# Kernel optimization log

Measured on AMD Instinct MI355X. Metric: run time of the kernel, lower is better.

Reference implementation:

```python
import jax, jax.numpy as jnp
import numpy as np

N_WORDS, N_SENTS = 200_000, 20_000
IN_DIM, OUT_DIM, FEAT = 128, 64, 50
N_EDGES = 2_000_000
NEG_SLOPE = 0.01  # torch F.leaky_relu default


def setup_inputs() -> dict:
    key = jax.random.key(0)
    k = jax.random.split(key, 7)
    h = jax.random.normal(k[0], (N_WORDS + N_SENTS, IN_DIM), dtype=jnp.float32)
    tfidf = jax.random.normal(k[1], (N_EDGES, FEAT), dtype=jnp.float32)
    W_fc = jax.random.normal(k[2], (OUT_DIM, IN_DIM), dtype=jnp.float32) / np.sqrt(IN_DIM)
    W_feat = jax.random.normal(k[3], (OUT_DIM, FEAT), dtype=jnp.float32) / np.sqrt(FEAT)
    W_attn = jax.random.normal(k[4], (1, 3 * OUT_DIM), dtype=jnp.float32) / np.sqrt(3 * OUT_DIM)
    src = jax.random.randint(k[5], (N_EDGES,), 0, N_WORDS, dtype=jnp.int32)
    dst = jax.random.randint(k[6], (N_EDGES,), 0, N_SENTS, dtype=jnp.int32)
    return {"h": h, "tfidf": tfidf, "W_fc": W_fc, "W_feat": W_feat,
            "W_attn": W_attn, "src": src, "dst": dst, "n_sents": N_SENTS}


def reference(h, tfidf, W_fc, W_feat, W_attn, src, dst, n_sents):
    n_words = h.shape[0] - n_sents
    out_dim = W_fc.shape[0]
    z = h @ W_fc.T                                  # [N, D]
    z_src = z[src]                                  # [E, D] gather word z
    z_dst = z[n_words + dst]                        # [E, D] gather sentence z
    dfeat = tfidf @ W_feat.T                        # [E, D] feat_fc
    wa = W_attn[0]                                  # [3D]; concat+linear == split dot
    e = z_src @ wa[:out_dim] + z_dst @ wa[out_dim:2 * out_dim] + dfeat @ wa[2 * out_dim:]
    e = jnp.where(e >= 0, e, NEG_SLOPE * e)         # leaky_relu, [E]
    # segment softmax over each sentence's incoming edges
    m = jax.ops.segment_max(e, dst, num_segments=n_sents)
    m = jnp.where(jnp.isfinite(m), m, 0.0)          # guard empty segments
    ex = jnp.exp(e - m[dst])
    denom = jax.ops.segment_sum(ex, dst, num_segments=n_sents)
    alpha = ex / denom[dst]                         # [E]
    # weighted scatter-sum of source features
    sh = jax.ops.segment_sum(alpha[:, None] * z_src, dst, num_segments=n_sents)
    return sh                                       # [n_sents, D]
```

## Files before the change

### kernel.cpp

```cpp
#include <hip/hip_runtime.h>
#include <hip/hip_bf16.h>
#include <hip/hip_fp16.h>
#include <cstdint>

#define IN_DIM 128
#define OUT_DIM 64
#define FEATD 50
#define NEG_SLOPE 0.01f

typedef unsigned int uint32;
typedef _Float16 half4 __attribute__((ext_vector_type(4)));
typedef float f32x4 __attribute__((ext_vector_type(4)));

__global__ __launch_bounds__(256) void k_v3zero(const float* __restrict__ W_feat,
                                                const float* __restrict__ W_attn,
                                                float* __restrict__ v3,
                                                uint32* __restrict__ cnt,
                                                int n_sents) {
  int i = blockIdx.x * 256 + threadIdx.x;
  if (i < n_sents) cnt[i] = 0u;
  if (blockIdx.x == 0 && threadIdx.x < FEATD) {
    int j = threadIdx.x;
    float s = 0.f;
    #pragma unroll
    for (int o = 0; o < OUT_DIM; ++o)
      s = fmaf(W_attn[2 * OUT_DIM + o], W_feat[o * FEATD + j], s);
    v3[j] = s;
  }
}

__global__ __launch_bounds__(256) void k_node_mfma(const float* __restrict__ h,
    const float* __restrict__ W_fc, const float* __restrict__ W_attn,
    __half* __restrict__ z, float* __restrict__ s1, float* __restrict__ s2,
    int n_words, int n_nodes) {
  __shared__ float zl[4][16][68];
  int w = threadIdx.x >> 6, lane = threadIdx.x & 63;
  int nb = blockIdx.x * 64 + w * 16;
  int lrow = lane & 15;
  int lk4 = (lane >> 4) * 4;

  int an = nb + lrow;
  if (an >= n_nodes) an = n_nodes - 1;
  const float* hrow = h + (size_t)an * IN_DIM;

  f32x4 acc[4];
  #pragma unroll
  for (int nt = 0; nt < 4; ++nt) acc[nt] = (f32x4){0.f, 0.f, 0.f, 0.f};

  #pragma unroll
  for (int ks = 0; ks < 8; ++ks) {
    float4 hv = *(const float4*)(hrow + ks * 16 + lk4);
    half4 a;
    a[0] = (_Float16)hv.x; a[1] = (_Float16)hv.y;
    a[2] = (_Float16)hv.z; a[3] = (_Float16)hv.w;
    #pragma unroll
    for (int nt = 0; nt < 4; ++nt) {
      const float* wrow = W_fc + (size_t)(nt * 16 + lrow) * IN_DIM + ks * 16 + lk4;
      float4 wv = *(const float4*)wrow;
      half4 b;
      b[0] = (_Float16)wv.x; b[1] = (_Float16)wv.y;
      b[2] = (_Float16)wv.z; b[3] = (_Float16)wv.w;
      acc[nt] = __builtin_amdgcn_mfma_f32_16x16x16f16(a, b, acc[nt], 0, 0, 0);
    }
  }

  int drow = (lane >> 4) * 4;
  #pragma unroll
  for (int nt = 0; nt < 4; ++nt)
    #pragma unroll
    for (int r = 0; r < 4; ++r)
      zl[w][drow + r][nt * 16 + lrow] = acc[nt][r];

  int node = lane >> 2;
  int chunk = lane & 3;
  float v[16];
  #pragma unroll
  for (int q = 0; q < 4; ++q) {
    float4 t = *(const float4*)&zl[w][node][chunk * 16 + q * 4];
    v[4 * q + 0] = t.x; v[4 * q + 1] = t.y;
    v[4 * q + 2] = t.z; v[4 * q + 3] = t.w;
  }

  int gn = nb + node;
  bool valid = gn < n_nodes;
  bool isword = gn < n_words;
  const float* wa = W_attn + (isword ? 0 : OUT_DIM) + chunk * 16;
  float p = 0.f;
  #pragma unroll
  for (int t = 0; t < 16; ++t) p = fmaf(v[t], wa[t], p);
  p += __shfl_xor(p, 1);
  p += __shfl_xor(p, 2);

  if (valid && chunk == 0) {
    if (isword) s1[gn] = p; else s2[gn - n_words] = p;
  }
  if (valid && isword) {
    uint32 d[8];
    #pragma unroll
    for (int k = 0; k < 8; ++k) {
      __half2 t = __floats2half2_rn(v[2 * k], v[2 * k + 1]);
      d[k] = *(uint32*)&t;
    }
    uint4* dst = (uint4*)(z + (size_t)gn * OUT_DIM + chunk * 16);
    dst[0] = make_uint4(d[0], d[1], d[2], d[3]);
    dst[1] = make_uint4(d[4], d[5], d[6], d[7]);
  }
}

__global__ __launch_bounds__(256) void k_hist(const int* __restrict__ dst,
                                              uint32* __restrict__ cnt,
                                              uint32* __restrict__ rank, int E) {
  int e = blockIdx.x * 256 + threadIdx.x;
  if (e < E) rank[e] = atomicAdd(&cnt[dst[e]], 1u);
}

__global__ __launch_bounds__(1024) void k_scan(const uint32* __restrict__ cnt,
    uint32* __restrict__ off, int n) {
  __shared__ uint32 part[1024];
  int t = threadIdx.x;
  int CH = (n + 1023) >> 10;
  int base = t * CH;
  uint32 s = 0;
  for (int k = 0; k < CH; ++k) { int i = base + k; if (i < n) s += cnt[i]; }
  part[t] = s;
  __syncthreads();
  uint32 x = s;
  for (int d = 1; d < 1024; d <<= 1) {
    uint32 v = (t >= d) ? part[t - d] : 0u;
    __syncthreads();
    x += v;
    part[t] = x;
    __syncthreads();
  }
  uint32 run = (t > 0) ? part[t - 1] : 0u;
  for (int k = 0; k < CH; ++k) {
    int i = base + k;
    if (i < n) { off[i] = run; run += cnt[i]; }
  }
  if (t == 1023) off[n] = part[1023];
}

__global__ __launch_bounds__(256) void k_edge(const float* __restrict__ tfidf,
    const int* __restrict__ src, const int* __restrict__ dst,
    const float* __restrict__ s1, const float* __restrict__ s2,
    const float* __restrict__ v3, const uint32* __restrict__ off,
    const uint32* __restrict__ rank, float2* __restrict__ pair, int E) {
  int e = blockIdx.x * 256 + threadIdx.x;
  if (e >= E) return;
  const float* row = tfidf + (size_t)e * FEATD;
  float f = 0.f;
  #pragma unroll
  for (int k = 0; k < FEATD / 2; ++k) {
    float2 v = *(const float2*)(row + 2 * k);
    f = fmaf(v.x, v3[2 * k], f);
    f = fmaf(v.y, v3[2 * k + 1], f);
  }
  int sidx = src[e], d = dst[e];
  float ev = s1[sidx] + s2[d] + f;
  ev = ev >= 0.f ? ev : NEG_SLOPE * ev;
  float exv = __expf(ev);
  float2 pr;
  pr.x = exv;
  pr.y = __int_as_float(sidx);
  pair[off[d] + rank[e]] = pr;
}

__global__ __launch_bounds__(256) void k_agg(const __half* __restrict__ z,
    const float2* __restrict__ pair, const uint32* __restrict__ off,
    float* __restrict__ out, int n_sents) {
  int w = threadIdx.x >> 6, lane = threadIdx.x & 63;
  int s = blockIdx.x * 4 + w;
  if (s >= n_sents) return;
  uint32 j0 = off[s], j1 = off[s + 1];

  float acc = 0.f, sa = 0.f;
  uint32 j = j0;
  for (; j + 8 <= j1; j += 8) {
    float2 p[8];
    #pragma unroll
    for (int k = 0; k < 8; ++k) p[k] = pair[j + k];
    float v[8];
    #pragma unroll
    for (int k = 0; k < 8; ++k)
      v[k] = __half2float(z[(size_t)(uint32)__float_as_int(p[k].y) * OUT_DIM + lane]);
    #pragma unroll
    for (int k = 0; k < 8; ++k) { acc = fmaf(p[k].x, v[k], acc); sa += p[k].x; }
  }
  for (; j + 4 <= j1; j += 4) {
    float2 p[4];
    #pragma unroll
    for (int k = 0; k < 4; ++k) p[k] = pair[j + k];
    float v[4];
    #pragma unroll
    for (int k = 0; k < 4; ++k)
      v[k] = __half2float(z[(size_t)(uint32)__float_as_int(p[k].y) * OUT_DIM + lane]);
    #pragma unroll
    for (int k = 0; k < 4; ++k) { acc = fmaf(p[k].x, v[k], acc); sa += p[k].x; }
  }
  for (; j < j1; ++j) {
    float2 p = pair[j];
    float v = __half2float(z[(size_t)(uint32)__float_as_int(p.y) * OUT_DIM + lane]);
    acc = fmaf(p.x, v, acc);
    sa += p.x;
  }

  out[(size_t)s * OUT_DIM + lane] = (sa > 0.f) ? (acc / sa) : 0.f;
}

extern "C" void kernel_launch(void* const* d_in, const int* in_sizes, int n_in,
                              void* d_out, int out_size, void* d_ws, size_t ws_size,
                              hipStream_t stream) {
  const float* h      = (const float*)d_in[0];
  const float* tfidf  = (const float*)d_in[1];
  const float* W_fc   = (const float*)d_in[2];
  const float* W_feat = (const float*)d_in[3];
  const float* W_attn = (const float*)d_in[4];
  const int*   src    = (const int*)d_in[5];
  const int*   dst    = (const int*)d_in[6];

  int n_nodes = in_sizes[0] / IN_DIM;
  int E       = in_sizes[5];
  int n_sents = out_size / OUT_DIM;
  int n_words = n_nodes - n_sents;
  float* out = (float*)d_out;

  char* ws = (char*)d_ws;
  size_t ofs = 0;
  auto alloc = [&](size_t bytes) -> char* {
    char* p = ws + ofs;
    ofs += (bytes + 255) / 256 * 256;
    return p;
  };
  __half* z      = (__half*)alloc((size_t)n_words * OUT_DIM * 2);
  float*  s1     = (float*)alloc((size_t)n_words * 4);
  float*  s2     = (float*)alloc((size_t)n_sents * 4);
  float2* pair   = (float2*)alloc((size_t)E * 8);
  uint32* rank   = (uint32*)alloc((size_t)E * 4);
  uint32* cnt    = (uint32*)alloc((size_t)n_sents * 4);
  uint32* offs   = (uint32*)alloc((size_t)(n_sents + 1) * 4);
  float*  v3     = (float*)alloc(FEATD * 4);
  (void)ws_size; (void)n_in;

  k_v3zero<<<(n_sents + 255) / 256, 256, 0, stream>>>(W_feat, W_attn, v3, cnt,
                                                      n_sents);
  k_node_mfma<<<(n_nodes + 63) / 64, 256, 0, stream>>>(h, W_fc, W_attn, z, s1,
                                                       s2, n_words, n_nodes);
  k_hist<<<(E + 255) / 256, 256, 0, stream>>>(dst, cnt, rank, E);
  k_scan<<<1, 1024, 0, stream>>>(cnt, offs, n_sents);
  k_edge<<<(E + 255) / 256, 256, 0, stream>>>(tfidf, src, dst, s1, s2, v3,
                                              offs, rank, pair, E);
  k_agg<<<(n_sents + 3) / 4, 256, 0, stream>>>(z, pair, offs, out, n_sents);
}
```

Measured before the change: 422.7 us.

## Fuse histogram into node GEMM launch and split edge dot across four lanes

Merges the dst histogram/rank atomics into the node MFMA kernel as extra blocks, so the two independent phases share one launch and can overlap. Each histogram thread now handles two edges with a vectorized int2 load. The edge kernel spreads each 50-wide tfidf dot product over four lanes with a shuffle reduction, so consecutive lanes read adjacent addresses instead of striding by 200 bytes. The cost is that three of every four lanes sit idle during the scatter tail, and the grid is four times larger.

```diff
diff --git a/kernel.cpp b/kernel.cpp
--- a/kernel.cpp
+++ b/kernel.cpp
@@ -29,11 +29,26 @@
   }
 }
 
-__global__ __launch_bounds__(256) void k_node_mfma(const float* __restrict__ h,
+__global__ __launch_bounds__(256) void k_node_hist(const float* __restrict__ h,
     const float* __restrict__ W_fc, const float* __restrict__ W_attn,
     __half* __restrict__ z, float* __restrict__ s1, float* __restrict__ s2,
-    int n_words, int n_nodes) {
+    const int* __restrict__ dst, uint32* __restrict__ cnt,
+    uint32* __restrict__ rank, int n_words, int n_nodes, int node_blocks,
+    int E) {
   __shared__ float zl[4][16][68];
+  if (blockIdx.x >= node_blocks) {
+    int i = (blockIdx.x - node_blocks) * 256 + threadIdx.x;
+    int e0 = i * 2;
+    if (e0 + 1 < E) {
+      int2 d2 = *(const int2*)(dst + e0);
+      uint32 r0 = atomicAdd(&cnt[d2.x], 1u);
+      uint32 r1 = atomicAdd(&cnt[d2.y], 1u);
+      *(uint2*)(rank + e0) = make_uint2(r0, r1);
+    } else if (e0 < E) {
+      rank[e0] = atomicAdd(&cnt[dst[e0]], 1u);
+    }
+    return;
+  }
   int w = threadIdx.x >> 6, lane = threadIdx.x & 63;
   int nb = blockIdx.x * 64 + w * 16;
   int lrow = lane & 15;
@@ -101,17 +116,10 @@
       __half2 t = __floats2half2_rn(v[2 * k], v[2 * k + 1]);
       d[k] = *(uint32*)&t;
     }
-    uint4* dst = (uint4*)(z + (size_t)gn * OUT_DIM + chunk * 16);
-    dst[0] = make_uint4(d[0], d[1], d[2], d[3]);
-    dst[1] = make_uint4(d[4], d[5], d[6], d[7]);
-  }
-}
-
-__global__ __launch_bounds__(256) void k_hist(const int* __restrict__ dst,
-                                              uint32* __restrict__ cnt,
-                                              uint32* __restrict__ rank, int E) {
-  int e = blockIdx.x * 256 + threadIdx.x;
-  if (e < E) rank[e] = atomicAdd(&cnt[dst[e]], 1u);
+    uint4* dstp = (uint4*)(z + (size_t)gn * OUT_DIM + chunk * 16);
+    dstp[0] = make_uint4(d[0], d[1], d[2], d[3]);
+    dstp[1] = make_uint4(d[4], d[5], d[6], d[7]);
+  }
 }
 
 __global__ __launch_bounds__(1024) void k_scan(const uint32* __restrict__ cnt,
@@ -145,24 +153,37 @@
     const float* __restrict__ s1, const float* __restrict__ s2,
     const float* __restrict__ v3, const uint32* __restrict__ off,
     const uint32* __restrict__ rank, float2* __restrict__ pair, int E) {
-  int e = blockIdx.x * 256 + threadIdx.x;
+  int t = threadIdx.x;
+  int g = t >> 2, r = t & 3;
+  int e = blockIdx.x * 64 + g;
   if (e >= E) return;
-  const float* row = tfidf + (size_t)e * FEATD;
+  const float2* row2 = (const float2*)(tfidf + (size_t)e * FEATD);
+  const float2* v32 = (const float2*)v3;
   float f = 0.f;
   #pragma unroll
-  for (int k = 0; k < FEATD / 2; ++k) {
-    float2 v = *(const float2*)(row + 2 * k);
-    f = fmaf(v.x, v3[2 * k], f);
-    f = fmaf(v.y, v3[2 * k + 1], f);
-  }
-  int sidx = src[e], d = dst[e];
-  float ev = s1[sidx] + s2[d] + f;
-  ev = ev >= 0.f ? ev : NEG_SLOPE * ev;
-  float exv = __expf(ev);
-  float2 pr;
-  pr.x = exv;
-  pr.y = __int_as_float(sidx);
-  pair[off[d] + rank[e]] = pr;
+  for (int q = 0; q < 6; ++q) {
+    float2 v = row2[r + 4 * q];
+    float2 c = v32[r + 4 * q];
+    f = fmaf(v.x, c.x, f);
+    f = fmaf(v.y, c.y, f);
+  }
+  if (r == 0) {
+    float2 v = row2[24];
+    float2 c = v32[24];
+    f = fmaf(v.x, c.x, f);
+    f = fmaf(v.y, c.y, f);
+  }
+  f += __shfl_xor(f, 1);
+  f += __shfl_xor(f, 2);
+  if (r == 0) {
+    int sidx = src[e], d = dst[e];
+    float ev = s1[sidx] + s2[d] + f;
+    ev = ev >= 0.f ? ev : NEG_SLOPE * ev;
+    float2 pr;
+    pr.x = __expf(ev);
+    pr.y = __int_as_float(sidx);
+    pair[off[d] + rank[e]] = pr;
+  }
 }
 
 __global__ __launch_bounds__(256) void k_agg(const __half* __restrict__ z,
@@ -241,13 +262,16 @@
   float*  v3     = (float*)alloc(FEATD * 4);
   (void)ws_size; (void)n_in;
 
+  int node_blocks = (n_nodes + 63) / 64;
+  int hist_blocks = (E + 511) / 512;
+
   k_v3zero<<<(n_sents + 255) / 256, 256, 0, stream>>>(W_feat, W_attn, v3, cnt,
                                                       n_sents);
-  k_node_mfma<<<(n_nodes + 63) / 64, 256, 0, stream>>>(h, W_fc, W_attn, z, s1,
-                                                       s2, n_words, n_nodes);
-  k_hist<<<(E + 255) / 256, 256, 0, stream>>>(dst, cnt, rank, E);
+  k_node_hist<<<node_blocks + hist_blocks, 256, 0, stream>>>(
+      h, W_fc, W_attn, z, s1, s2, dst, cnt, rank, n_words, n_nodes,
+      node_blocks, E);
   k_scan<<<1, 1024, 0, stream>>>(cnt, offs, n_sents);
-  k_edge<<<(E + 255) / 256, 256, 0, stream>>>(tfidf, src, dst, s1, s2, v3,
-                                              offs, rank, pair, E);
+  k_edge<<<(E + 63) / 64, 256, 0, stream>>>(tfidf, src, dst, s1, s2, v3,
+                                            offs, rank, pair, E);
   k_agg<<<(n_sents + 3) / 4, 256, 0, stream>>>(z, pair, offs, out, n_sents);
 }
```

Result: no change. 430.5 us (+1.8%).

## Split aggregation into source-sorted scatter of weighted rows and contiguous reduce

Applied to the files above, without the earlier changes.

Edges are additionally bucketed by source word, so each word's z row is loaded once and multiplied by its edge weights. The weighted rows are scattered into a per-edge half buffer ordered by destination, which the sentence reduction then reads contiguously. This is meant to replace random z gathers in aggregation with streaming reads. In exchange it adds a second atomic histogram and scan, and a very large intermediate buffer that must be written and read.

```diff
diff --git a/kernel.cpp b/kernel.cpp
--- a/kernel.cpp
+++ b/kernel.cpp
@@ -12,13 +12,15 @@
 typedef _Float16 half4 __attribute__((ext_vector_type(4)));
 typedef float f32x4 __attribute__((ext_vector_type(4)));
 
-__global__ __launch_bounds__(256) void k_v3zero(const float* __restrict__ W_feat,
-                                                const float* __restrict__ W_attn,
-                                                float* __restrict__ v3,
-                                                uint32* __restrict__ cnt,
-                                                int n_sents) {
+__global__ __launch_bounds__(256) void k_init(const float* __restrict__ W_feat,
+                                              const float* __restrict__ W_attn,
+                                              float* __restrict__ v3,
+                                              uint32* __restrict__ cnt_d,
+                                              uint32* __restrict__ cnt_s,
+                                              int n_sents, int n_words) {
   int i = blockIdx.x * 256 + threadIdx.x;
-  if (i < n_sents) cnt[i] = 0u;
+  if (i < n_sents) cnt_d[i] = 0u;
+  if (i < n_words) cnt_s[i] = 0u;
   if (blockIdx.x == 0 && threadIdx.x < FEATD) {
     int j = threadIdx.x;
     float s = 0.f;
@@ -101,21 +103,32 @@
       __half2 t = __floats2half2_rn(v[2 * k], v[2 * k + 1]);
       d[k] = *(uint32*)&t;
     }
-    uint4* dst = (uint4*)(z + (size_t)gn * OUT_DIM + chunk * 16);
-    dst[0] = make_uint4(d[0], d[1], d[2], d[3]);
-    dst[1] = make_uint4(d[4], d[5], d[6], d[7]);
-  }
-}
-
-__global__ __launch_bounds__(256) void k_hist(const int* __restrict__ dst,
-                                              uint32* __restrict__ cnt,
-                                              uint32* __restrict__ rank, int E) {
+    uint4* dstp = (uint4*)(z + (size_t)gn * OUT_DIM + chunk * 16);
+    dstp[0] = make_uint4(d[0], d[1], d[2], d[3]);
+    dstp[1] = make_uint4(d[4], d[5], d[6], d[7]);
+  }
+}
+
+__global__ __launch_bounds__(256) void k_hist2(const int* __restrict__ dst,
+                                               const int* __restrict__ src,
+                                               uint32* __restrict__ cnt_d,
+                                               uint32* __restrict__ cnt_s,
+                                               uint32* __restrict__ rank_d,
+                                               uint32* __restrict__ rank_s,
+                                               int E) {
   int e = blockIdx.x * 256 + threadIdx.x;
-  if (e < E) rank[e] = atomicAdd(&cnt[dst[e]], 1u);
-}
-
-__global__ __launch_bounds__(1024) void k_scan(const uint32* __restrict__ cnt,
-    uint32* __restrict__ off, int n) {
+  if (e < E) {
+    rank_d[e] = atomicAdd(&cnt_d[dst[e]], 1u);
+    rank_s[e] = atomicAdd(&cnt_s[src[e]], 1u);
+  }
+}
+
+__global__ __launch_bounds__(1024) void k_scan2(const uint32* __restrict__ cnt_d,
+    uint32* __restrict__ off_d, int nd, const uint32* __restrict__ cnt_s,
+    uint32* __restrict__ off_s, int ns) {
+  const uint32* cnt = (blockIdx.x == 0) ? cnt_d : cnt_s;
+  uint32* off = (blockIdx.x == 0) ? off_d : off_s;
+  int n = (blockIdx.x == 0) ? nd : ns;
   __shared__ uint32 part[1024];
   int t = threadIdx.x;
   int CH = (n + 1023) >> 10;
@@ -143,8 +156,10 @@
 __global__ __launch_bounds__(256) void k_edge(const float* __restrict__ tfidf,
     const int* __restrict__ src, const int* __restrict__ dst,
     const float* __restrict__ s1, const float* __restrict__ s2,
-    const float* __restrict__ v3, const uint32* __restrict__ off,
-    const uint32* __restrict__ rank, float2* __restrict__ pair, int E) {
+    const float* __restrict__ v3, const uint32* __restrict__ off_d,
+    const uint32* __restrict__ off_s, const uint32* __restrict__ rank_d,
+    const uint32* __restrict__ rank_s, float* __restrict__ aw,
+    float2* __restrict__ asd, int E) {
   int e = blockIdx.x * 256 + threadIdx.x;
   if (e >= E) return;
   const float* row = tfidf + (size_t)e * FEATD;
@@ -159,51 +174,62 @@
   float ev = s1[sidx] + s2[d] + f;
   ev = ev >= 0.f ? ev : NEG_SLOPE * ev;
   float exv = __expf(ev);
+  uint32 sd = off_d[d] + rank_d[e];
+  uint32 ss = off_s[sidx] + rank_s[e];
+  aw[sd] = exv;
   float2 pr;
   pr.x = exv;
-  pr.y = __int_as_float(sidx);
-  pair[off[d] + rank[e]] = pr;
-}
-
-__global__ __launch_bounds__(256) void k_agg(const __half* __restrict__ z,
-    const float2* __restrict__ pair, const uint32* __restrict__ off,
+  pr.y = __int_as_float((int)sd);
+  asd[ss] = pr;
+}
+
+__global__ __launch_bounds__(256) void k_pv(const __half* __restrict__ z,
+    const float2* __restrict__ asd, const uint32* __restrict__ off_s,
+    __half* __restrict__ wbuf, int n_words) {
+  int w = blockIdx.x * 4 + (threadIdx.x >> 6);
+  int lane = threadIdx.x & 63;
+  if (w >= n_words) return;
+  float zv = __half2float(z[(size_t)w * OUT_DIM + lane]);
+  uint32 j0 = off_s[w], j1 = off_s[w + 1];
+  uint32 j = j0;
+  for (; j + 2 <= j1; j += 2) {
+    float2 a0 = asd[j];
+    float2 a1 = asd[j + 1];
+    uint32 t0 = (uint32)__float_as_int(a0.y);
+    uint32 t1 = (uint32)__float_as_int(a1.y);
+    wbuf[(size_t)t0 * OUT_DIM + lane] = __float2half(a0.x * zv);
+    wbuf[(size_t)t1 * OUT_DIM + lane] = __float2half(a1.x * zv);
+  }
+  if (j < j1) {
+    float2 a0 = asd[j];
+    uint32 t0 = (uint32)__float_as_int(a0.y);
+    wbuf[(size_t)t0 * OUT_DIM + lane] = __float2half(a0.x * zv);
+  }
+}
+
+__global__ __launch_bounds__(256) void k_aggB(const __half* __restrict__ wbuf,
+    const float* __restrict__ aw, const uint32* __restrict__ off_d,
     float* __restrict__ out, int n_sents) {
-  int w = threadIdx.x >> 6, lane = threadIdx.x & 63;
-  int s = blockIdx.x * 4 + w;
+  int s = blockIdx.x * 4 + (threadIdx.x >> 6);
+  int lane = threadIdx.x & 63;
   if (s >= n_sents) return;
-  uint32 j0 = off[s], j1 = off[s + 1];
-
+  uint32 j0 = off_d[s], j1 = off_d[s + 1];
   float acc = 0.f, sa = 0.f;
   uint32 j = j0;
   for (; j + 8 <= j1; j += 8) {
-    float2 p[8];
-    #pragma unroll
-    for (int k = 0; k < 8; ++k) p[k] = pair[j + k];
-    float v[8];
-    #pragma unroll
-    for (int k = 0; k < 8; ++k)
-      v[k] = __half2float(z[(size_t)(uint32)__float_as_int(p[k].y) * OUT_DIM + lane]);
-    #pragma unroll
-    for (int k = 0; k < 8; ++k) { acc = fmaf(p[k].x, v[k], acc); sa += p[k].x; }
-  }
-  for (; j + 4 <= j1; j += 4) {
-    float2 p[4];
-    #pragma unroll
-    for (int k = 0; k < 4; ++k) p[k] = pair[j + k];
-    float v[4];
-    #pragma unroll
-    for (int k = 0; k < 4; ++k)
-      v[k] = __half2float(z[(size_t)(uint32)__float_as_int(p[k].y) * OUT_DIM + lane]);
-    #pragma unroll
-    for (int k = 0; k < 4; ++k) { acc = fmaf(p[k].x, v[k], acc); sa += p[k].x; }
+    __half hv[8];
+    float av[8];
+    #pragma unroll
+    for (int k = 0; k < 8; ++k) hv[k] = wbuf[(size_t)(j + k) * OUT_DIM + lane];
+    #pragma unroll
+    for (int k = 0; k < 8; ++k) av[k] = aw[j + k];
+    #pragma unroll
+    for (int k = 0; k < 8; ++k) { acc += __half2float(hv[k]); sa += av[k]; }
   }
   for (; j < j1; ++j) {
-    float2 p = pair[j];
-    float v = __half2float(z[(size_t)(uint32)__float_as_int(p.y) * OUT_DIM + lane]);
-    acc = fmaf(p.x, v, acc);
-    sa += p.x;
-  }
-
+    acc += __half2float(wbuf[(size_t)j * OUT_DIM + lane]);
+    sa += aw[j];
+  }
   out[(size_t)s * OUT_DIM + lane] = (sa > 0.f) ? (acc / sa) : 0.f;
 }
 
@@ -234,20 +260,28 @@
   __half* z      = (__half*)alloc((size_t)n_words * OUT_DIM * 2);
   float*  s1     = (float*)alloc((size_t)n_words * 4);
   float*  s2     = (float*)alloc((size_t)n_sents * 4);
-  float2* pair   = (float2*)alloc((size_t)E * 8);
-  uint32* rank   = (uint32*)alloc((size_t)E * 4);
-  uint32* cnt    = (uint32*)alloc((size_t)n_sents * 4);
-  uint32* offs   = (uint32*)alloc((size_t)(n_sents + 1) * 4);
+  __half* wbuf   = (__half*)alloc((size_t)E * OUT_DIM * 2);
+  float2* asd    = (float2*)alloc((size_t)E * 8);
+  float*  aw     = (float*)alloc((size_t)E * 4);
+  uint32* rank_d = (uint32*)alloc((size_t)E * 4);
+  uint32* rank_s = (uint32*)alloc((size_t)E * 4);
+  uint32* cnt_d  = (uint32*)alloc((size_t)n_sents * 4);
+  uint32* cnt_s  = (uint32*)alloc((size_t)n_words * 4);
+  uint32* off_d  = (uint32*)alloc((size_t)(n_sents + 1) * 4);
+  uint32* off_s  = (uint32*)alloc((size_t)(n_words + 1) * 4);
   float*  v3     = (float*)alloc(FEATD * 4);
   (void)ws_size; (void)n_in;
 
-  k_v3zero<<<(n_sents + 255) / 256, 256, 0, stream>>>(W_feat, W_attn, v3, cnt,
-                                                      n_sents);
+  k_init<<<(n_words + 255) / 256, 256, 0, stream>>>(W_feat, W_attn, v3, cnt_d,
+                                                    cnt_s, n_sents, n_words);
   k_node_mfma<<<(n_nodes + 63) / 64, 256, 0, stream>>>(h, W_fc, W_attn, z, s1,
                                                        s2, n_words, n_nodes);
-  k_hist<<<(E + 255) / 256, 256, 0, stream>>>(dst, cnt, rank, E);
-  k_scan<<<1, 1024, 0, stream>>>(cnt, offs, n_sents);
+  k_hist2<<<(E + 255) / 256, 256, 0, stream>>>(dst, src, cnt_d, cnt_s, rank_d,
+                                               rank_s, E);
+  k_scan2<<<2, 1024, 0, stream>>>(cnt_d, off_d, n_sents, cnt_s, off_s, n_words);
   k_edge<<<(E + 255) / 256, 256, 0, stream>>>(tfidf, src, dst, s1, s2, v3,
-                                              offs, rank, pair, E);
-  k_agg<<<(n_sents + 3) / 4, 256, 0, stream>>>(z, pair, offs, out, n_sents);
-}
+                                              off_d, off_s, rank_d, rank_s,
+                                              aw, asd, E);
+  k_pv<<<(n_words + 3) / 4, 256, 0, stream>>>(z, asd, off_s, wbuf, n_words);
+  k_aggB<<<(n_sents + 3) / 4, 256, 0, stream>>>(wbuf, aw, off_d, out, n_sents);
+}
```

New measurement: 994.2 us. 2.35x slower.
